# Performance work log

Hardware: AMD Instinct MI355X
Metric: run time of the kernel (lower is better)

The kernel has to match this reference:

```python
import jax, jax.numpy as jnp
import numpy as np

F = 8          # number of tables/features
B = 4096       # batch size (number of bags per feature)
V = 100000     # rows per embedding table
D = 128        # embedding dim
N = 81920      # total jagged values per feature (avg bag length ~20)


def setup_inputs() -> dict:
    key = jax.random.key(0)
    k_vals, k_offs, k_tab = jax.random.split(key, 3)
    # jagged indices into each table: [F, N]
    values = jax.random.randint(k_vals, (F, N), 0, V, dtype=jnp.int32)
    # offsets with include_last_offset=True: [F, B+1], nondecreasing, offs[0]=0, offs[-1]=N
    inner = jnp.sort(jax.random.randint(k_offs, (F, B - 1), 0, N + 1, dtype=jnp.int32), axis=1)
    offsets = jnp.concatenate(
        [jnp.zeros((F, 1), jnp.int32), inner, jnp.full((F, 1), N, jnp.int32)], axis=1
    )
    # embedding tables: [F, V, D]
    tables = jax.random.normal(k_tab, (F, V, D), dtype=jnp.float32)
    return {"values": values, "offsets": offsets, "tables": tables}


def reference(values, offsets, tables):
    """EmbeddingBagCollection forward: per-feature EmbeddingBag(sum) + concat.

    values:  [F, N] int32 indices
    offsets: [F, B+1] int32 (include_last_offset)
    tables:  [F, V, D] float32
    returns: [B, F*D] pooled embeddings (KeyedTensor.values())
    """
    pos = jnp.arange(N)

    def per_feature(vals, offs, table):
        # bag id for each value: index of the bag whose [offs[i], offs[i+1]) contains pos
        seg = jnp.searchsorted(offs, pos, side="right") - 1  # [N] in [0, B-1]
        gathered = table[vals]                               # [N, D]
        return jax.ops.segment_sum(gathered, seg, num_segments=B)  # [B, D]

    pooled = jax.vmap(per_feature)(values, offsets, tables)  # [F, B, D]
    return jnp.transpose(pooled, (1, 0, 2)).reshape(B, F * D)
```

## Files before the change

kernel.cpp:

```cpp
#include <hip/hip_runtime.h>

#define FF 8
#define BB 4096
#define VV 100000
#define DD 128
#define NN 81920

__global__ __launch_bounds__(256, 8) void ebc_pool_kernel(
    const int* __restrict__ values,
    const int* __restrict__ offsets,
    const float* __restrict__ tables,
    float* __restrict__ out)
{
    const int wave = threadIdx.x >> 6;
    const int lane = threadIdx.x & 63;
    const int half = lane >> 5;
    const int hl   = lane & 31;
    const int gbag = blockIdx.x * 4 + wave;
    const int f = gbag >> 12;
    const int b = gbag & (BB - 1);

    const int* __restrict__ offs = offsets + f * (BB + 1);
    const int start = offs[b];
    const int end   = offs[b + 1];

    const int* __restrict__ vals = values + f * NN;
    const float* __restrict__ tab = tables + (size_t)f * VV * DD;

    float4 acc = make_float4(0.f, 0.f, 0.f, 0.f);

    int i = start;
    for (; i + 4 <= end; i += 4) {
        const int i0 = vals[i + 0];
        const int i1 = vals[i + 1];
        const int i2 = vals[i + 2];
        const int i3 = vals[i + 3];
        const int r0 = half ? i1 : i0;
        const int r1 = half ? i3 : i2;
        const float4 v0 = ((const float4*)(tab + (size_t)r0 * DD))[hl];
        const float4 v1 = ((const float4*)(tab + (size_t)r1 * DD))[hl];
        acc.x += v0.x + v1.x;
        acc.y += v0.y + v1.y;
        acc.z += v0.z + v1.z;
        acc.w += v0.w + v1.w;
    }
    for (; i < end; i += 2) {
        const int ii = i + half;
        if (ii < end) {
            const int r = vals[ii];
            const float4 v = ((const float4*)(tab + (size_t)r * DD))[hl];
            acc.x += v.x;
            acc.y += v.y;
            acc.z += v.z;
            acc.w += v.w;
        }
    }

    acc.x += __shfl_xor(acc.x, 32, 64);
    acc.y += __shfl_xor(acc.y, 32, 64);
    acc.z += __shfl_xor(acc.z, 32, 64);
    acc.w += __shfl_xor(acc.w, 32, 64);

    if (half == 0) {
        float4* __restrict__ o =
            (float4*)(out + (size_t)b * (FF * DD) + f * DD);
        o[hl] = acc;
    }
}

extern "C" void kernel_launch(void* const* d_in, const int* in_sizes, int n_in,
                              void* d_out, int out_size, void* d_ws, size_t ws_size,
                              hipStream_t stream) {
    const int*   values  = (const int*)d_in[0];
    const int*   offsets = (const int*)d_in[1];
    const float* tables  = (const float*)d_in[2];
    float*       out     = (float*)d_out;

    const int total_bags = FF * BB;
    const int blocks = total_bags / 4;
    ebc_pool_kernel<<<blocks, 256, 0, stream>>>(values, offsets, tables, out);
}
```

Measured before the change: 527.7 us.

## Load bag indices cooperatively and issue eight row gathers per step

Each wave now loads up to 64 indices of its bag in one coalesced load and broadcasts them with readlane. Every lane then covers a float2 of the 128-wide row, so a full wave reads one row instead of two half-waves reading two. Eight row loads are issued per inner step, with zero weights masking the tail, to raise memory-level parallelism. Blocks are remapped so consecutive blocks cover different features for the same bags, which writes output rows closer together. The masked tail still loads row of index 0 redundantly, and the per-lane load width drops from float4 to float2.

```diff
diff --git a/kernel.cpp b/kernel.cpp
--- a/kernel.cpp
+++ b/kernel.cpp
@@ -14,58 +14,46 @@
 {
     const int wave = threadIdx.x >> 6;
     const int lane = threadIdx.x & 63;
-    const int half = lane >> 5;
-    const int hl   = lane & 31;
-    const int gbag = blockIdx.x * 4 + wave;
-    const int f = gbag >> 12;
-    const int b = gbag & (BB - 1);
+
+    const int f = blockIdx.x & 7;
+    const int b = ((blockIdx.x >> 3) << 2) + wave;
 
     const int* __restrict__ offs = offsets + f * (BB + 1);
-    const int start = offs[b];
-    const int end   = offs[b + 1];
+    const int start = __builtin_amdgcn_readfirstlane(offs[b]);
+    const int end   = __builtin_amdgcn_readfirstlane(offs[b + 1]);
 
     const int* __restrict__ vals = values + f * NN;
-    const float* __restrict__ tab = tables + (size_t)f * VV * DD;
+    const float* __restrict__ tab = tables + (size_t)f * (VV * DD);
 
-    float4 acc = make_float4(0.f, 0.f, 0.f, 0.f);
+    float ax = 0.f, ay = 0.f;
 
-    int i = start;
-    for (; i + 4 <= end; i += 4) {
-        const int i0 = vals[i + 0];
-        const int i1 = vals[i + 1];
-        const int i2 = vals[i + 2];
-        const int i3 = vals[i + 3];
-        const int r0 = half ? i1 : i0;
-        const int r1 = half ? i3 : i2;
-        const float4 v0 = ((const float4*)(tab + (size_t)r0 * DD))[hl];
-        const float4 v1 = ((const float4*)(tab + (size_t)r1 * DD))[hl];
-        acc.x += v0.x + v1.x;
-        acc.y += v0.y + v1.y;
-        acc.z += v0.z + v1.z;
-        acc.w += v0.w + v1.w;
-    }
-    for (; i < end; i += 2) {
-        const int ii = i + half;
-        if (ii < end) {
-            const int r = vals[ii];
-            const float4 v = ((const float4*)(tab + (size_t)r * DD))[hl];
-            acc.x += v.x;
-            acc.y += v.y;
-            acc.z += v.z;
-            acc.w += v.w;
+    for (int i0 = start; i0 < end; i0 += 64) {
+        int g = i0 + lane;
+        g = (g < end) ? g : (end - 1);
+        const int idxv = vals[g];
+
+        const int rem = end - i0;
+        const int nr = (rem < 64) ? rem : 64;
+
+        for (int r = 0; r < nr; r += 8) {
+#define EBC_ROW(k)                                                          \
+            const int   in##k = (r + k) < nr;                               \
+            const int   rr##k = in##k ? (r + k) : 0;                        \
+            const float w##k  = in##k ? 1.f : 0.f;                          \
+            const int   s##k  = __builtin_amdgcn_readlane(idxv, rr##k);     \
+            const float2 v##k = *((const float2*)(tab + (size_t)s##k * DD) + lane);
+            EBC_ROW(0) EBC_ROW(1) EBC_ROW(2) EBC_ROW(3)
+            EBC_ROW(4) EBC_ROW(5) EBC_ROW(6) EBC_ROW(7)
+#undef EBC_ROW
+            ax += ((w0 * v0.x + w1 * v1.x) + (w2 * v2.x + w3 * v3.x)) +
+                  ((w4 * v4.x + w5 * v5.x) + (w6 * v6.x + w7 * v7.x));
+            ay += ((w0 * v0.y + w1 * v1.y) + (w2 * v2.y + w3 * v3.y)) +
+                  ((w4 * v4.y + w5 * v5.y) + (w6 * v6.y + w7 * v7.y));
         }
     }
 
-    acc.x += __shfl_xor(acc.x, 32, 64);
-    acc.y += __shfl_xor(acc.y, 32, 64);
-    acc.z += __shfl_xor(acc.z, 32, 64);
-    acc.w += __shfl_xor(acc.w, 32, 64);
-
-    if (half == 0) {
-        float4* __restrict__ o =
-            (float4*)(out + (size_t)b * (FF * DD) + f * DD);
-        o[hl] = acc;
-    }
+    float2* __restrict__ o = (float2*)(out + (size_t)b * (FF * DD) + f * DD);
+    o[lane] = make_float2(ax, ay);
 }
 
 extern "C" void kernel_launch(void* const* d_in, const int* in_sizes, int n_in,
```

New measurement: 526.7 us. About the same (-0.2%).
